# Optimization experiments

Hardware: AMD Instinct MI355X
Metric: run time of the kernel (lower is better)

Reference implementation:

```python
import jax, jax.numpy as jnp
import numpy as np

N = 50000       # nodes
DEG = 16        # out-degree per node
E = N * DEG     # edges
IN_F = 128
OUT_F = 64
NO_NETWORKS = 2
ALPHA = 0.2     # leakyrelu negative slope


def setup_inputs() -> dict:
    key = jax.random.key(0)
    k_h, k_w, k_a, k_nw = jax.random.split(key, 4)
    h = jax.random.normal(k_h, (N, IN_F), dtype=jnp.float32)
    # xavier-ish scales matching nn.init.xavier_uniform_(gain=1.414)
    W = jax.random.normal(k_w, (IN_F, OUT_F), dtype=jnp.float32) * float(np.sqrt(2.0 / (IN_F + OUT_F)))
    a = jax.random.normal(k_a, (2 * NO_NETWORKS * OUT_F, 1), dtype=jnp.float32) * float(np.sqrt(2.0 / (2 * NO_NETWORKS * OUT_F + 1)))
    nw = jax.random.normal(k_nw, (NO_NETWORKS, 1), dtype=jnp.float32)
    # deterministic unique edges: node i -> (i+1..DEG) mod N; no duplicates,
    # so torch coalesce() would only merge the two networks' shared edge set.
    src = np.repeat(np.arange(N, dtype=np.int64), DEG)
    dst = (src + np.tile(np.arange(1, DEG + 1, dtype=np.int64), N)) % N
    edge_index = jnp.asarray(np.stack([src, dst], axis=0))  # [2, E]
    return {"h": h, "edge_index": edge_index, "W": W, "a": a, "nw": nw}


def reference(h, edge_index, W, a, nw):
    wts = jax.nn.softmax(nw, axis=0)          # [K,1], softmax over networks
    Wh = h @ W                                 # [N, OUT_F]
    src, dst = edge_index[0], edge_index[1]    # [E], [E]
    vals = jnp.zeros((edge_index.shape[1],), dtype=Wh.dtype)
    for i in range(NO_NETWORKS):
        a1 = a[2 * i * OUT_F:(2 * i + 1) * OUT_F, 0]        # [OUT_F]
        a2 = a[(2 * i + 1) * OUT_F:(2 * i + 2) * OUT_F, 0]  # [OUT_F]
        Wh1 = Wh @ a1                                        # [N]
        Wh2 = Wh @ a2                                        # [N]
        e = Wh1[src] + Wh2[dst]                              # [E]
        lrelu = jnp.where(e > 0, e, ALPHA * e)               # leakyrelu
        # NOTE: original code uses wts[0] for every network (faithful bug)
        vals = vals + wts[0, 0] * jnp.exp(-lrelu)
    # coalesce of the two identical edge sets == per-edge sum (done above);
    # F.softmax over the flat coalesced values (global softmax over all edges)
    vals = jax.nn.softmax(vals)
    # sparse @ Wh: h_prime[i] = sum_{e: src[e]==i} vals[e] * Wh[dst[e]]
    h_prime = jax.ops.segment_sum(vals[:, None] * Wh[dst], src, num_segments=N)
    return jax.nn.elu(h_prime)  # concat=True path
```

## Files before the change

kernel.cpp:

```cpp
#include <hip/hip_runtime.h>
#include <math.h>

#define N_NODES 50000
#define DEG 16
#define NE (N_NODES * DEG)
#define IN_F 128
#define OUT_F 64
#define ALPHA 0.2f
#define NB_EDGE (NE / 256)

#define BM 64
#define HPAD (IN_F + 4)
#define NBLK ((N_NODES + BM - 1) / BM)

__device__ __forceinline__ int edge_dst(int e) {
    int t = (e >> 4) + 1 + (e & 15);
    return t >= N_NODES ? t - N_NODES : t;
}


#define FMAS(a0, a1, a2, a3, hs, wv) \
    a0 = fmaf(hs, wv.x, a0);         \
    a1 = fmaf(hs, wv.y, a1);         \
    a2 = fmaf(hs, wv.z, a2);         \
    a3 = fmaf(hs, wv.w, a3);

#define ROWFMA(r, hv)                                      \
    FMAS(acc##r##0, acc##r##1, acc##r##2, acc##r##3, hv.x, w0) \
    FMAS(acc##r##0, acc##r##1, acc##r##2, acc##r##3, hv.y, w1) \
    FMAS(acc##r##0, acc##r##1, acc##r##2, acc##r##3, hv.z, w2) \
    FMAS(acc##r##0, acc##r##1, acc##r##2, acc##r##3, hv.w, w3)

__global__ __launch_bounds__(256) void gemm_kernel(
    const float* __restrict__ h, const float* __restrict__ W,
    const float* __restrict__ a,
    float* __restrict__ Wh, float* __restrict__ s1, float* __restrict__ s2)
{
    __shared__ float Wlds[IN_F * OUT_F];
    __shared__ float hlds[BM * HPAD];

    const int tid = threadIdx.x;
    const int tx = tid & 15;
    const int ty = tid >> 4;
    const int row0 = blockIdx.x * BM;

    for (int i = tid; i < IN_F * OUT_F / 4; i += 256)
        ((float4*)Wlds)[i] = ((const float4*)W)[i];

    for (int i = tid; i < BM * IN_F / 4; i += 256) {
        const int r  = i >> 5;
        const int c4 = i & 31;
        int gr = row0 + r;
        if (gr >= N_NODES) gr = N_NODES - 1;
        const float4 v = ((const float4*)(h + (size_t)gr * IN_F))[c4];
        *(float4*)(hlds + r * HPAD + c4 * 4) = v;
    }

    const float4 av0 = *(const float4*)(a +   0 + tx * 4);
    const float4 av1 = *(const float4*)(a +  64 + tx * 4);
    const float4 av2 = *(const float4*)(a + 128 + tx * 4);
    const float4 av3 = *(const float4*)(a + 192 + tx * 4);

    __syncthreads();

    float acc00 = 0.f, acc01 = 0.f, acc02 = 0.f, acc03 = 0.f;
    float acc10 = 0.f, acc11 = 0.f, acc12 = 0.f, acc13 = 0.f;
    float acc20 = 0.f, acc21 = 0.f, acc22 = 0.f, acc23 = 0.f;
    float acc30 = 0.f, acc31 = 0.f, acc32 = 0.f, acc33 = 0.f;

    const float* hbase = hlds + (ty * 4) * HPAD;
    const float* wbase = Wlds + tx * 4;

    #pragma unroll 8
    for (int k4 = 0; k4 < IN_F / 4; ++k4) {
        const float4 h0 = *(const float4*)(hbase + 0 * HPAD + k4 * 4);
        const float4 h1 = *(const float4*)(hbase + 1 * HPAD + k4 * 4);
        const float4 h2 = *(const float4*)(hbase + 2 * HPAD + k4 * 4);
        const float4 h3 = *(const float4*)(hbase + 3 * HPAD + k4 * 4);
        const float4 w0 = *(const float4*)(wbase + (k4 * 4 + 0) * OUT_F);
        const float4 w1 = *(const float4*)(wbase + (k4 * 4 + 1) * OUT_F);
        const float4 w2 = *(const float4*)(wbase + (k4 * 4 + 2) * OUT_F);
        const float4 w3 = *(const float4*)(wbase + (k4 * 4 + 3) * OUT_F);

        ROWFMA(0, h0)
        ROWFMA(1, h1)
        ROWFMA(2, h2)
        ROWFMA(3, h3)
    }

    {
        const int g0 = row0 + ty * 4;
        if (g0 + 0 < N_NODES) *(float4*)(Wh + (size_t)(g0 + 0) * OUT_F + tx * 4) = make_float4(acc00, acc01, acc02, acc03);
        if (g0 + 1 < N_NODES) *(float4*)(Wh + (size_t)(g0 + 1) * OUT_F + tx * 4) = make_float4(acc10, acc11, acc12, acc13);
        if (g0 + 2 < N_NODES) *(float4*)(Wh + (size_t)(g0 + 2) * OUT_F + tx * 4) = make_float4(acc20, acc21, acc22, acc23);
        if (g0 + 3 < N_NODES) *(float4*)(Wh + (size_t)(g0 + 3) * OUT_F + tx * 4) = make_float4(acc30, acc31, acc32, acc33);
    }

#define PROJ(r)                                                                          \
    {                                                                                    \
        const int grow = row0 + ty * 4 + r;                                              \
        float p0 = acc##r##0 * av0.x + acc##r##1 * av0.y + acc##r##2 * av0.z + acc##r##3 * av0.w; \
        float p1 = acc##r##0 * av1.x + acc##r##1 * av1.y + acc##r##2 * av1.z + acc##r##3 * av1.w; \
        float p2 = acc##r##0 * av2.x + acc##r##1 * av2.y + acc##r##2 * av2.z + acc##r##3 * av2.w; \
        float p3 = acc##r##0 * av3.x + acc##r##1 * av3.y + acc##r##2 * av3.z + acc##r##3 * av3.w; \
        p0 += __shfl_xor(p0, 8); p0 += __shfl_xor(p0, 4); p0 += __shfl_xor(p0, 2); p0 += __shfl_xor(p0, 1); \
        p1 += __shfl_xor(p1, 8); p1 += __shfl_xor(p1, 4); p1 += __shfl_xor(p1, 2); p1 += __shfl_xor(p1, 1); \
        p2 += __shfl_xor(p2, 8); p2 += __shfl_xor(p2, 4); p2 += __shfl_xor(p2, 2); p2 += __shfl_xor(p2, 1); \
        p3 += __shfl_xor(p3, 8); p3 += __shfl_xor(p3, 4); p3 += __shfl_xor(p3, 2); p3 += __shfl_xor(p3, 1); \
        if (tx == 0 && grow < N_NODES) {                                                 \
            s1[grow] = p0;                                                               \
            s2[grow] = p1;                                                               \
            s1[N_NODES + grow] = p2;                                                     \
            s2[N_NODES + grow] = p3;                                                     \
        }                                                                                \
    }
    PROJ(0)
    PROJ(1)
    PROJ(2)
    PROJ(3)
#undef PROJ
}

__global__ __launch_bounds__(256) void edge_kernel(
    const float* __restrict__ s1, const float* __restrict__ s2,
    const float* __restrict__ nw,
    float* __restrict__ vals, float* __restrict__ pmax, float* __restrict__ psum)
{
    const int e = blockIdx.x * 256 + threadIdx.x;
    const int wv = threadIdx.x >> 6;
    const int lane = threadIdx.x & 63;

    const float n0 = nw[0], n1 = nw[1];
    const float nm = fmaxf(n0, n1);
    const float w00 = expf(n0 - nm) / (expf(n0 - nm) + expf(n1 - nm));

    const int src = e >> 4;
    const int dst = edge_dst(e);
    const float e0 = s1[src] + s2[dst];
    const float l0 = e0 > 0.f ? e0 : ALPHA * e0;
    const float e1 = s1[N_NODES + src] + s2[N_NODES + dst];
    const float l1 = e1 > 0.f ? e1 : ALPHA * e1;
    const float v = w00 * (expf(-l0) + expf(-l1));
    vals[e] = v;

    float wm = v;
    #pragma unroll
    for (int off = 32; off > 0; off >>= 1) wm = fmaxf(wm, __shfl_xor(wm, off));
    __shared__ float smax[4];
    if (lane == 0) smax[wv] = wm;
    __syncthreads();
    const float bmax = fmaxf(fmaxf(smax[0], smax[1]), fmaxf(smax[2], smax[3]));

    float se = expf(v - bmax);
    #pragma unroll
    for (int off = 32; off > 0; off >>= 1) se += __shfl_xor(se, off);
    __shared__ float ssum[4];
    if (lane == 0) ssum[wv] = se;
    __syncthreads();
    if (threadIdx.x == 0) {
        pmax[blockIdx.x] = bmax;
        psum[blockIdx.x] = ssum[0] + ssum[1] + ssum[2] + ssum[3];
    }
}

__global__ __launch_bounds__(1024) void finalize_kernel(
    const float* __restrict__ pmax, const float* __restrict__ psum,
    float* __restrict__ gstats)
{
    const int tid = threadIdx.x;
    const int wv = tid >> 6, lane = tid & 63;

    float m = -1e30f;
    for (int i = tid; i < NB_EDGE; i += 1024) m = fmaxf(m, pmax[i]);
    #pragma unroll
    for (int off = 32; off > 0; off >>= 1) m = fmaxf(m, __shfl_xor(m, off));
    __shared__ float sm[16];
    if (lane == 0) sm[wv] = m;
    __syncthreads();
    float gmax = sm[0];
    #pragma unroll
    for (int i = 1; i < 16; ++i) gmax = fmaxf(gmax, sm[i]);

    float s = 0.f;
    for (int i = tid; i < NB_EDGE; i += 1024) s += psum[i] * expf(pmax[i] - gmax);
    #pragma unroll
    for (int off = 32; off > 0; off >>= 1) s += __shfl_xor(s, off);
    __shared__ float ss[16];
    if (lane == 0) ss[wv] = s;
    __syncthreads();
    if (tid == 0) {
        float t = 0.f;
        #pragma unroll
        for (int i = 0; i < 16; ++i) t += ss[i];
        gstats[0] = gmax;
        gstats[1] = 1.0f / t;
    }
}

__global__ __launch_bounds__(256) void aggregate_kernel(
    const float* __restrict__ Wh, const float* __restrict__ vals,
    const float* __restrict__ gstats, float* __restrict__ out)
{
    const int wv = threadIdx.x >> 6, lane = threadIdx.x & 63;
    const int node = blockIdx.x * 4 + wv;
    const float gmax = gstats[0], inv = gstats[1];
    const int ebase = node * DEG;

    float p = 0.f;
    if (lane < DEG) p = expf(vals[ebase + lane] - gmax) * inv;

    float acc = 0.f;
    #pragma unroll
    for (int j = 0; j < DEG; ++j) {
        const float pj = __shfl(p, j);
        int dj = node + 1 + j;
        if (dj >= N_NODES) dj -= N_NODES;
        acc = fmaf(pj, Wh[(size_t)dj * OUT_F + lane], acc);
    }
    out[(size_t)node * OUT_F + lane] = acc > 0.f ? acc : expf(acc) - 1.f;
}

extern "C" void kernel_launch(void* const* d_in, const int* in_sizes, int n_in,
                              void* d_out, int out_size, void* d_ws, size_t ws_size,
                              hipStream_t stream) {
    const float* h  = (const float*)d_in[0];
    const float* W  = (const float*)d_in[2];
    const float* a  = (const float*)d_in[3];
    const float* nw = (const float*)d_in[4];
    float* out = (float*)d_out;

    float* ws     = (float*)d_ws;
    float* Wh     = ws;
    float* s1     = Wh + (size_t)N_NODES * OUT_F;
    float* s2     = s1 + 2 * N_NODES;
    float* vals   = s2 + 2 * N_NODES;
    float* pmax   = vals + NE;
    float* psum   = pmax + NB_EDGE;
    float* gstats = psum + NB_EDGE;

    gemm_kernel<<<NBLK, 256, 0, stream>>>(h, W, a, Wh, s1, s2);
    edge_kernel<<<NB_EDGE, 256, 0, stream>>>(s1, s2, nw, vals, pmax, psum);
    finalize_kernel<<<1, 1024, 0, stream>>>(pmax, psum, gstats);
    aggregate_kernel<<<N_NODES / 4, 256, 0, stream>>>(Wh, vals, gstats, out);
}
```

Baseline: 120.7 us.

## Defer global softmax normalization and fuse edge scoring into aggregation

Removes the max-subtracted global softmax pipeline (edge, finalize and aggregate kernels). A per-node kernel now computes the unnormalized exp scores for its 16 edges, aggregates Wh with them, and atomically adds their sum to one global denominator. A final elementwise kernel divides by that sum and applies ELU. This drops the per-edge vals buffer and the single-block finalize kernel. In exchange it writes and re-reads an intermediate U array, funnels one atomic per block into a single address, and loses the max-subtraction overflow guard.

```diff
diff --git a/kernel.cpp b/kernel.cpp
--- a/kernel.cpp
+++ b/kernel.cpp
@@ -7,16 +7,10 @@
 #define IN_F 128
 #define OUT_F 64
 #define ALPHA 0.2f
-#define NB_EDGE (NE / 256)
 
 #define BM 64
 #define HPAD (IN_F + 4)
 #define NBLK ((N_NODES + BM - 1) / BM)
-
-__device__ __forceinline__ int edge_dst(int e) {
-    int t = (e >> 4) + 1 + (e & 15);
-    return t >= N_NODES ? t - N_NODES : t;
-}
 
 
 #define FMAS(a0, a1, a2, a3, hs, wv) \
@@ -25,7 +19,7 @@
     a2 = fmaf(hs, wv.z, a2);         \
     a3 = fmaf(hs, wv.w, a3);
 
-#define ROWFMA(r, hv)                                      \
+#define ROWFMA(r, hv)                                          \
     FMAS(acc##r##0, acc##r##1, acc##r##2, acc##r##3, hv.x, w0) \
     FMAS(acc##r##0, acc##r##1, acc##r##2, acc##r##3, hv.y, w1) \
     FMAS(acc##r##0, acc##r##1, acc##r##2, acc##r##3, hv.z, w2) \
@@ -34,7 +28,8 @@
 __global__ __launch_bounds__(256) void gemm_kernel(
     const float* __restrict__ h, const float* __restrict__ W,
     const float* __restrict__ a,
-    float* __restrict__ Wh, float* __restrict__ s1, float* __restrict__ s2)
+    float* __restrict__ Wh, float* __restrict__ s1, float* __restrict__ s2,
+    float* __restrict__ gsum)
 {
     __shared__ float Wlds[IN_F * OUT_F];
     __shared__ float hlds[BM * HPAD];
@@ -43,6 +38,8 @@
     const int tx = tid & 15;
     const int ty = tid >> 4;
     const int row0 = blockIdx.x * BM;
+
+    if (blockIdx.x == 0 && tid == 0) gsum[0] = 0.f;
 
     for (int i = tid; i < IN_F * OUT_F / 4; i += 256)
         ((float4*)Wlds)[i] = ((const float4*)W)[i];
@@ -121,103 +118,60 @@
 #undef PROJ
 }
 
-__global__ __launch_bounds__(256) void edge_kernel(
+__global__ __launch_bounds__(256) void node_kernel(
     const float* __restrict__ s1, const float* __restrict__ s2,
-    const float* __restrict__ nw,
-    float* __restrict__ vals, float* __restrict__ pmax, float* __restrict__ psum)
+    const float* __restrict__ nw, const float* __restrict__ Wh,
+    float* __restrict__ U, float* __restrict__ gsum)
 {
-    const int e = blockIdx.x * 256 + threadIdx.x;
-    const int wv = threadIdx.x >> 6;
-    const int lane = threadIdx.x & 63;
+    const int wv = threadIdx.x >> 6, lane = threadIdx.x & 63;
+    const int node = blockIdx.x * 4 + wv;
 
     const float n0 = nw[0], n1 = nw[1];
     const float nm = fmaxf(n0, n1);
     const float w00 = expf(n0 - nm) / (expf(n0 - nm) + expf(n1 - nm));
 
-    const int src = e >> 4;
-    const int dst = edge_dst(e);
-    const float e0 = s1[src] + s2[dst];
-    const float l0 = e0 > 0.f ? e0 : ALPHA * e0;
-    const float e1 = s1[N_NODES + src] + s2[N_NODES + dst];
-    const float l1 = e1 > 0.f ? e1 : ALPHA * e1;
-    const float v = w00 * (expf(-l0) + expf(-l1));
-    vals[e] = v;
+    float p = 0.f;
+    if (lane < DEG) {
+        int dj = node + 1 + lane;
+        if (dj >= N_NODES) dj -= N_NODES;
+        const float e0 = s1[node] + s2[dj];
+        const float l0 = e0 > 0.f ? e0 : ALPHA * e0;
+        const float e1 = s1[N_NODES + node] + s2[N_NODES + dj];
+        const float l1 = e1 > 0.f ? e1 : ALPHA * e1;
+        p = expf(w00 * (expf(-l0) + expf(-l1)));
+    }
 
-    float wm = v;
-    #pragma unroll
-    for (int off = 32; off > 0; off >>= 1) wm = fmaxf(wm, __shfl_xor(wm, off));
-    __shared__ float smax[4];
-    if (lane == 0) smax[wv] = wm;
-    __syncthreads();
-    const float bmax = fmaxf(fmaxf(smax[0], smax[1]), fmaxf(smax[2], smax[3]));
-
-    float se = expf(v - bmax);
-    #pragma unroll
-    for (int off = 32; off > 0; off >>= 1) se += __shfl_xor(se, off);
-    __shared__ float ssum[4];
-    if (lane == 0) ssum[wv] = se;
-    __syncthreads();
-    if (threadIdx.x == 0) {
-        pmax[blockIdx.x] = bmax;
-        psum[blockIdx.x] = ssum[0] + ssum[1] + ssum[2] + ssum[3];
-    }
-}
-
-__global__ __launch_bounds__(1024) void finalize_kernel(
-    const float* __restrict__ pmax, const float* __restrict__ psum,
-    float* __restrict__ gstats)
-{
-    const int tid = threadIdx.x;
-    const int wv = tid >> 6, lane = tid & 63;
-
-    float m = -1e30f;
-    for (int i = tid; i < NB_EDGE; i += 1024) m = fmaxf(m, pmax[i]);
-    #pragma unroll
-    for (int off = 32; off > 0; off >>= 1) m = fmaxf(m, __shfl_xor(m, off));
-    __shared__ float sm[16];
-    if (lane == 0) sm[wv] = m;
-    __syncthreads();
-    float gmax = sm[0];
-    #pragma unroll
-    for (int i = 1; i < 16; ++i) gmax = fmaxf(gmax, sm[i]);
-
-    float s = 0.f;
-    for (int i = tid; i < NB_EDGE; i += 1024) s += psum[i] * expf(pmax[i] - gmax);
-    #pragma unroll
-    for (int off = 32; off > 0; off >>= 1) s += __shfl_xor(s, off);
-    __shared__ float ss[16];
-    if (lane == 0) ss[wv] = s;
-    __syncthreads();
-    if (tid == 0) {
-        float t = 0.f;
-        #pragma unroll
-        for (int i = 0; i < 16; ++i) t += ss[i];
-        gstats[0] = gmax;
-        gstats[1] = 1.0f / t;
-    }
-}
-
-__global__ __launch_bounds__(256) void aggregate_kernel(
-    const float* __restrict__ Wh, const float* __restrict__ vals,
-    const float* __restrict__ gstats, float* __restrict__ out)
-{
-    const int wv = threadIdx.x >> 6, lane = threadIdx.x & 63;
-    const int node = blockIdx.x * 4 + wv;
-    const float gmax = gstats[0], inv = gstats[1];
-    const int ebase = node * DEG;
-
-    float p = 0.f;
-    if (lane < DEG) p = expf(vals[ebase + lane] - gmax) * inv;
-
-    float acc = 0.f;
+    float acc = 0.f, t = 0.f;
     #pragma unroll
     for (int j = 0; j < DEG; ++j) {
         const float pj = __shfl(p, j);
         int dj = node + 1 + j;
         if (dj >= N_NODES) dj -= N_NODES;
         acc = fmaf(pj, Wh[(size_t)dj * OUT_F + lane], acc);
+        t += pj;
     }
-    out[(size_t)node * OUT_F + lane] = acc > 0.f ? acc : expf(acc) - 1.f;
+    U[(size_t)node * OUT_F + lane] = acc;
+
+    __shared__ float tp[4];
+    if (lane == 0) tp[wv] = t;
+    __syncthreads();
+    if (threadIdx.x == 0)
+        atomicAdd(gsum, tp[0] + tp[1] + tp[2] + tp[3]);
+}
+
+__global__ __launch_bounds__(256) void norm_kernel(
+    const float* __restrict__ U, const float* __restrict__ gsum,
+    float* __restrict__ out)
+{
+    const float inv = 1.0f / gsum[0];
+    const size_t i = (size_t)blockIdx.x * 256 + threadIdx.x;
+    const float4 u = ((const float4*)U)[i];
+    float4 o;
+    const float x = u.x * inv; o.x = x > 0.f ? x : expf(x) - 1.f;
+    const float y = u.y * inv; o.y = y > 0.f ? y : expf(y) - 1.f;
+    const float z = u.z * inv; o.z = z > 0.f ? z : expf(z) - 1.f;
+    const float w = u.w * inv; o.w = w > 0.f ? w : expf(w) - 1.f;
+    ((float4*)out)[i] = o;
 }
 
 extern "C" void kernel_launch(void* const* d_in, const int* in_sizes, int n_in,
@@ -229,17 +183,14 @@
     const float* nw = (const float*)d_in[4];
     float* out = (float*)d_out;
 
-    float* ws     = (float*)d_ws;
-    float* Wh     = ws;
-    float* s1     = Wh + (size_t)N_NODES * OUT_F;
-    float* s2     = s1 + 2 * N_NODES;
-    float* vals   = s2 + 2 * N_NODES;
-    float* pmax   = vals + NE;
-    float* psum   = pmax + NB_EDGE;
-    float* gstats = psum + NB_EDGE;
+    float* ws   = (float*)d_ws;
+    float* Wh   = ws;
+    float* U    = Wh + (size_t)N_NODES * OUT_F;
+    float* s1   = U  + (size_t)N_NODES * OUT_F;
+    float* s2   = s1 + 2 * N_NODES;
+    float* gsum = s2 + 2 * N_NODES;
 
-    gemm_kernel<<<NBLK, 256, 0, stream>>>(h, W, a, Wh, s1, s2);
-    edge_kernel<<<NB_EDGE, 256, 0, stream>>>(s1, s2, nw, vals, pmax, psum);
-    finalize_kernel<<<1, 1024, 0, stream>>>(pmax, psum, gstats);
-    aggregate_kernel<<<N_NODES / 4, 256, 0, stream>>>(Wh, vals, gstats, out);
+    gemm_kernel<<<NBLK, 256, 0, stream>>>(h, W, a, Wh, s1, s2, gsum);
+    node_kernel<<<N_NODES / 4, 256, 0, stream>>>(s1, s2, nw, Wh, U, gsum);
+    norm_kernel<<<(N_NODES * OUT_F) / (256 * 4), 256, 0, stream>>>(U, gsum, out);
 }
```

After: 264.9 us. 119% more time.
